# Performance work log

Measured on AMD Instinct MI355X. Metric: run time of the kernel, lower is better.

## Reference

```python
import jax, jax.numpy as jnp
import numpy as np

D_IN = 1024
D_OUT = 1024
NUM_HEADS = 16
HEAD_DIM = D_OUT // NUM_HEADS


def setup_inputs() -> dict:
    key = jax.random.key(0)
    ks = jax.random.split(key, 6)
    s = 1.0 / np.sqrt(D_IN)
    x = jax.random.normal(ks[0], (2, 2048, D_IN), dtype=jnp.float32)
    Wq = jax.random.uniform(ks[1], (D_IN, D_OUT), jnp.float32, -s, s)
    Wk = jax.random.uniform(ks[2], (D_IN, D_OUT), jnp.float32, -s, s)
    Wv = jax.random.uniform(ks[3], (D_IN, D_OUT), jnp.float32, -s, s)
    Wo = jax.random.uniform(ks[4], (D_OUT, D_OUT), jnp.float32, -s, s)
    bo = jax.random.uniform(ks[5], (D_OUT,), jnp.float32, -s, s)
    return {"x": x, "Wq": Wq, "Wk": Wk, "Wv": Wv, "Wo": Wo, "bo": bo}


def reference(x, Wq, Wk, Wv, Wo, bo):
    b, s, _ = x.shape
    # Note: source assigns keys = W_query(x), queries = W_key(x) (swapped names);
    # replicate exactly.
    keys = (x @ Wq).reshape(b, s, NUM_HEADS, HEAD_DIM)
    values = (x @ Wv).reshape(b, s, NUM_HEADS, HEAD_DIM)
    queries = (x @ Wk).reshape(b, s, NUM_HEADS, HEAD_DIM)
    # [b, h, q, k] attention scores; source's masked_fill is non in-place and
    # discarded, so NO causal mask is applied (faithful to the bug).
    scores = jnp.einsum("bqhd,bkhd->bhqk", queries, keys)
    attn = jax.nn.softmax(scores / np.sqrt(HEAD_DIM), axis=-1)
    # dropout p=0.0 -> identity
    ctx = jnp.einsum("bhqk,bkhd->bqhd", attn, values).reshape(b, s, D_OUT)
    return ctx @ Wo + bo
```

## Files before the change

kernel.cpp:

```cpp
#include <hip/hip_runtime.h>
#include <math.h>

#define DI 1024
#define SQ 2048
#define NB 2
#define NH 16
#define HD 64
#define QSCALE 0.18033688f

typedef __attribute__((ext_vector_type(8))) short short8;
typedef __attribute__((ext_vector_type(4))) float f32x4;
typedef __attribute__((ext_vector_type(2))) unsigned int uint2v;
typedef __attribute__((ext_vector_type(4))) int int4v;
typedef __attribute__((ext_vector_type(4))) unsigned short ushort4v;

static __device__ __forceinline__ unsigned short f2bf(float f) {
    union { float f; unsigned u; } v; v.f = f;
    unsigned r = v.u + 0x7FFFu + ((v.u >> 16) & 1u);
    return (unsigned short)(r >> 16);
}
static __device__ __forceinline__ float fexp2(float x) {
    float r; asm("v_exp_f32 %0, %1" : "=v"(r) : "v"(x)); return r;
}
static __device__ __forceinline__ unsigned cvtpk(float lo, float hi) {
    unsigned r; asm("v_cvt_pk_bf16_f32 %0, %1, %2" : "=v"(r) : "v"(lo), "v"(hi)); return r;
}

typedef __attribute__((address_space(1))) const unsigned int gas_uint;
typedef __attribute__((address_space(3))) unsigned int las_uint;
static __device__ __forceinline__ void gload16(const void* g, void* l) {
    __builtin_amdgcn_global_load_lds((gas_uint*)g, (las_uint*)l, 16, 0, 0);
}

#define MFMA16(a, b, c) __builtin_amdgcn_mfma_f32_16x16x32_bf16(a, b, c, 0, 0, 0)

__global__ __launch_bounds__(256) void k_cvt_bf16(const float* __restrict__ src,
                                                  unsigned short* __restrict__ dst) {
    int i = blockIdx.x * 256 + threadIdx.x;
    const f32x4* s4 = (const f32x4*)src + (size_t)i * 2;
    f32x4 a = s4[0], b = s4[1];
    ushort4v o0, o1;
    o0[0] = f2bf(a[0]); o0[1] = f2bf(a[1]); o0[2] = f2bf(a[2]); o0[3] = f2bf(a[3]);
    o1[0] = f2bf(b[0]); o1[1] = f2bf(b[1]); o1[2] = f2bf(b[2]); o1[3] = f2bf(b[3]);
    *(ushort4v*)(dst + (size_t)i * 8)     = o0;
    *(ushort4v*)(dst + (size_t)i * 8 + 4) = o1;
}

__global__ __launch_bounds__(256) void k_transpose_w4(const float* __restrict__ W0, const float* __restrict__ W1,
                                                      const float* __restrict__ W2, const float* __restrict__ W3,
                                                      unsigned short* __restrict__ T0, unsigned short* __restrict__ T1,
                                                      unsigned short* __restrict__ T2, unsigned short* __restrict__ T3) {
    const float* W; unsigned short* T;
    switch (blockIdx.z) {
        case 0: W = W0; T = T0; break;
        case 1: W = W1; T = T1; break;
        case 2: W = W2; T = T2; break;
        default: W = W3; T = T3; break;
    }
    __shared__ float t[32][33];
    int tx = threadIdx.x, ty = threadIdx.y;
    int n0 = blockIdx.x * 32, k0 = blockIdx.y * 32;
#pragma unroll
    for (int j = 0; j < 32; j += 8) t[ty + j][tx] = W[(size_t)(k0 + ty + j) * DI + n0 + tx];
    __syncthreads();
#pragma unroll
    for (int j = 0; j < 32; j += 8)
        T[(size_t)(n0 + ty + j) * DI + k0 + tx] = f2bf(t[tx][ty + j]);
}

template <int MODE>
__global__ __launch_bounds__(256) void k_gemm(const unsigned short* __restrict__ A,
                                              const unsigned short* __restrict__ Bt,
                                              unsigned short* __restrict__ oK,
                                              unsigned short* __restrict__ oQ,
                                              unsigned short* __restrict__ oV,
                                              const float* __restrict__ bias) {
    __shared__ __align__(16) unsigned short As[2][128 * 32];
    __shared__ __align__(16) unsigned short Bs[2][128 * 32];
    const int tid = threadIdx.x, lane = tid & 63, w = tid >> 6;
    const int wr = w >> 1, wc = w & 1;
    const int tm = blockIdx.y, tn = blockIdx.x;
    const unsigned short* Abase = A  + (size_t)tm * 128 * DI;
    const unsigned short* Bbase = Bt + (size_t)tn * 128 * DI;

    auto stage = [&](int kt, int bi) {
#pragma unroll
        for (int i = 0; i < 2; ++i) {
            int u = tid + i * 256;
            int row = u >> 2, c8 = (u & 3) * 8;
            gload16(Abase + (size_t)row * DI + kt * 32 + c8, &As[bi][u * 8]);
            gload16(Bbase + (size_t)row * DI + kt * 32 + c8, &Bs[bi][u * 8]);
        }
    };

    f32x4 acc[4][4] = {};
    stage(0, 0);
    for (int kt = 0; kt < DI / 32; ++kt) {
        __syncthreads();
        if (kt + 1 < DI / 32) stage(kt + 1, (kt + 1) & 1);
        const int bi = kt & 1;
        short8 af[4], bf[4];
#pragma unroll
        for (int mi = 0; mi < 4; ++mi)
            af[mi] = *(const short8*)&As[bi][(wr * 64 + mi * 16 + (lane & 15)) * 32 + (lane >> 4) * 8];
#pragma unroll
        for (int ni = 0; ni < 4; ++ni)
            bf[ni] = *(const short8*)&Bs[bi][(wc * 64 + ni * 16 + (lane & 15)) * 32 + (lane >> 4) * 8];
        __builtin_amdgcn_s_setprio(1);
#pragma unroll
        for (int mi = 0; mi < 4; ++mi)
#pragma unroll
            for (int ni = 0; ni < 4; ++ni)
                acc[mi][ni] = MFMA16(af[mi], bf[ni], acc[mi][ni]);
        __builtin_amdgcn_s_setprio(0);
    }

    if (MODE == 2) {
        float bv[4];
#pragma unroll
        for (int ni = 0; ni < 4; ++ni) bv[ni] = bias[tn * 128 + wc * 64 + ni * 16 + (lane & 15)];
        float* Co = (float*)oK;
#pragma unroll
        for (int mi = 0; mi < 4; ++mi)
#pragma unroll
            for (int ni = 0; ni < 4; ++ni)
#pragma unroll
                for (int j = 0; j < 4; ++j) {
                    int m = tm * 128 + wr * 64 + mi * 16 + (lane >> 4) * 4 + j;
                    int n = tn * 128 + wc * 64 + ni * 16 + (lane & 15);
                    Co[(size_t)m * DI + n] = acc[mi][ni][j] + bv[ni];
                }
    } else {
        const int which = tn >> 3;
        if (which < 2) {
            unsigned short* Co = which ? oQ : oK;
            const float scl = which ? QSCALE : 1.0f;
#pragma unroll
            for (int mi = 0; mi < 4; ++mi)
#pragma unroll
                for (int ni = 0; ni < 4; ++ni)
#pragma unroll
                    for (int j = 0; j < 4; ++j) {
                        int m = tm * 128 + wr * 64 + mi * 16 + (lane >> 4) * 4 + j;
                        int n = (tn & 7) * 128 + wc * 64 + ni * 16 + (lane & 15);
                        Co[(((size_t)(m >> 11) * NH + (n >> 6)) * SQ + (m & 2047)) * HD + (n & 63)] =
                            f2bf(acc[mi][ni][j] * scl);
                    }
        } else {
#pragma unroll
            for (int mi = 0; mi < 4; ++mi)
#pragma unroll
                for (int ni = 0; ni < 4; ++ni) {
                    uint2v pk;
                    pk[0] = cvtpk(acc[mi][ni][0], acc[mi][ni][1]);
                    pk[1] = cvtpk(acc[mi][ni][2], acc[mi][ni][3]);
                    int m = tm * 128 + wr * 64 + mi * 16 + (lane >> 4) * 4;
                    int n = (tn & 7) * 128 + wc * 64 + ni * 16 + (lane & 15);
                    *(uint2v*)&oV[(((size_t)(m >> 11) * NH + (n >> 6)) * HD + (n & 63)) * SQ + (m & 2047)] = pk;
                }
        }
    }
}

__global__ __launch_bounds__(256) void k_attn(const unsigned short* __restrict__ Q,
                                              const unsigned short* __restrict__ K,
                                              const unsigned short* __restrict__ Vt,
                                              unsigned short* __restrict__ ctx) {
    __shared__ __align__(16) unsigned short Ks[2][64 * 64];
    __shared__ __align__(16) unsigned short Vs[2][64 * 64];
    __shared__ __align__(16) unsigned short Ps[4][32 * 64];
    const int tid = threadIdx.x, lane = tid & 63, w = tid >> 6;
    const int bh = blockIdx.y;
    const int q0 = blockIdx.x * 128;
    const unsigned short* qh = Q  + (size_t)bh * SQ * HD;
    const unsigned short* kh = K  + (size_t)bh * SQ * HD;
    const unsigned short* vh = Vt + (size_t)bh * HD * SQ;

    short8 qf[2][2];
#pragma unroll
    for (int mi = 0; mi < 2; ++mi)
#pragma unroll
        for (int kk = 0; kk < 2; ++kk)
            qf[mi][kk] = *(const short8*)(qh + (size_t)(q0 + w * 32 + mi * 16 + (lane & 15)) * HD +
                                          kk * 32 + (lane >> 4) * 8);

    f32x4 o[2][4] = {};
    float ls[2][4] = {};

    auto stage = [&](int kt, int bi) {
#pragma unroll
        for (int i = 0; i < 2; ++i) {
            int u = tid + i * 256;
            int row = u >> 3, c = u & 7;
            int cs = c ^ (row & 7);
            gload16(kh + (size_t)(kt * 64 + row) * HD + cs * 8, &Ks[bi][u * 8]);
            gload16(vh + (size_t)row * SQ + kt * 64 + cs * 8, &Vs[bi][u * 8]);
        }
    };

    stage(0, 0);
    for (int kt = 0; kt < SQ / 64; ++kt) {
        __syncthreads();
        if (kt + 1 < SQ / 64) stage(kt + 1, (kt + 1) & 1);
        const int bi = kt & 1;

        f32x4 s[2][4] = {};
#pragma unroll
        for (int kk = 0; kk < 2; ++kk) {
            short8 kb[4];
#pragma unroll
            for (int ni = 0; ni < 4; ++ni)
                kb[ni] = *(const short8*)&Ks[bi][(ni * 16 + (lane & 15)) * 64 +
                                                 (((kk * 4 + (lane >> 4)) ^ (lane & 7)) * 8)];
            __builtin_amdgcn_s_setprio(1);
#pragma unroll
            for (int mi = 0; mi < 2; ++mi)
#pragma unroll
                for (int ni = 0; ni < 4; ++ni)
                    s[mi][ni] = MFMA16(qf[mi][kk], kb[ni], s[mi][ni]);
            __builtin_amdgcn_s_setprio(0);
        }

#pragma unroll
        for (int mi = 0; mi < 2; ++mi)
#pragma unroll
            for (int ni = 0; ni < 4; ++ni) {
                float p0 = fexp2(s[mi][ni][0]), p1 = fexp2(s[mi][ni][1]);
                float p2 = fexp2(s[mi][ni][2]), p3 = fexp2(s[mi][ni][3]);
                ls[mi][0] += p0; ls[mi][1] += p1; ls[mi][2] += p2; ls[mi][3] += p3;
                unsigned pk01 = cvtpk(p0, p1), pk23 = cvtpk(p2, p3);
                int colc = ni * 2 + ((lane & 15) >> 3);
                int cl = lane & 7;
#pragma unroll
                for (int j = 0; j < 4; ++j) {
                    int row = mi * 16 + (lane >> 4) * 4 + j;
                    unsigned v = (j & 1) ? ((j < 2 ? pk01 : pk23) >> 16)
                                         : (j < 2 ? pk01 : pk23);
                    Ps[w][row * 64 + ((colc ^ (row & 7)) * 8) + cl] = (unsigned short)v;
                }
            }

#pragma unroll
        for (int kk = 0; kk < 2; ++kk) {
            short8 pa[2], vb[4];
#pragma unroll
            for (int mi = 0; mi < 2; ++mi) {
                int row = mi * 16 + (lane & 15);
                pa[mi] = *(const short8*)&Ps[w][row * 64 + (((kk * 4 + (lane >> 4)) ^ (row & 7)) * 8)];
            }
#pragma unroll
            for (int ni = 0; ni < 4; ++ni)
                vb[ni] = *(const short8*)&Vs[bi][(ni * 16 + (lane & 15)) * 64 +
                                                 (((kk * 4 + (lane >> 4)) ^ (lane & 7)) * 8)];
            __builtin_amdgcn_s_setprio(1);
#pragma unroll
            for (int mi = 0; mi < 2; ++mi)
#pragma unroll
                for (int ni = 0; ni < 4; ++ni)
                    o[mi][ni] = MFMA16(pa[mi], vb[ni], o[mi][ni]);
            __builtin_amdgcn_s_setprio(0);
        }
    }

    float inv[2][4];
#pragma unroll
    for (int mi = 0; mi < 2; ++mi)
#pragma unroll
        for (int j = 0; j < 4; ++j) {
            float v = ls[mi][j];
            v += __shfl_xor(v, 1); v += __shfl_xor(v, 2);
            v += __shfl_xor(v, 4); v += __shfl_xor(v, 8);
            inv[mi][j] = 1.0f / v;
        }

    const int b = bh >> 4, h = bh & 15;
#pragma unroll
    for (int mi = 0; mi < 2; ++mi)
#pragma unroll
        for (int ni = 0; ni < 4; ++ni)
#pragma unroll
            for (int j = 0; j < 4; ++j) {
                int q = q0 + w * 32 + mi * 16 + (lane >> 4) * 4 + j;
                int col = h * 64 + ni * 16 + (lane & 15);
                ctx[((size_t)(b * SQ + q)) * DI + col] = f2bf(o[mi][ni][j] * inv[mi][j]);
            }
}

extern "C" void kernel_launch(void* const* d_in, const int* in_sizes, int n_in,
                              void* d_out, int out_size, void* d_ws, size_t ws_size,
                              hipStream_t stream) {
    const float* x  = (const float*)d_in[0];
    const float* Wq = (const float*)d_in[1];
    const float* Wk = (const float*)d_in[2];
    const float* Wv = (const float*)d_in[3];
    const float* Wo = (const float*)d_in[4];
    const float* bo = (const float*)d_in[5];

    char* ws = (char*)d_ws;
    unsigned short* xb   = (unsigned short*)(ws);
    unsigned short* Wall = (unsigned short*)(ws + (8u  << 20));
    unsigned short* Wot  = (unsigned short*)(ws + (14u << 20));
    unsigned short* Qh   = (unsigned short*)(ws + (16u << 20));
    unsigned short* Kh   = (unsigned short*)(ws + (24u << 20));
    unsigned short* Vt   = (unsigned short*)(ws + (32u << 20));
    unsigned short* ctx  = (unsigned short*)(ws + (40u << 20));

    k_cvt_bf16<<<2048, 256, 0, stream>>>(x, xb);
    k_transpose_w4<<<dim3(32, 32, 4), dim3(32, 8), 0, stream>>>(
        Wq, Wk, Wv, Wo, Wall, Wall + (1u << 20), Wall + (2u << 20), Wot);

    k_gemm<0><<<dim3(24, 32), 256, 0, stream>>>(xb, Wall, Kh, Qh, Vt, nullptr);

    k_attn<<<dim3(16, 32), 256, 0, stream>>>(Qh, Kh, Vt, ctx);

    k_gemm<2><<<dim3(8, 32), 256, 0, stream>>>(ctx, Wot, (unsigned short*)d_out, nullptr, nullptr, bo);
}
```

Before: 134.6 us.

## Rewrite attention with 32x32 MFMA, register-resident P via permlane swap

The attention kernel now uses 32x32x16 bf16 MFMAs and computes S transposed (K as A operand), so the exponentiated probabilities can be repacked into the PV operand in registers using v_permlane32_swap instead of round-tripping through a per-wave LDS P buffer. The row-sum reduction shrinks to one cross-half shuffle. Output is staged through LDS for coalesced 16-byte ctx stores, and the 1D grid is remapped so consecutive blocks spread across heads, likely for XCD/L2 locality. This removes LDS writes and reads of P and scattered 2-byte global stores, at the cost of more complex lane mapping and register pressure from 16-wide accumulators.

```diff
diff --git a/kernel.cpp b/kernel.cpp
--- a/kernel.cpp
+++ b/kernel.cpp
@@ -10,6 +10,7 @@
 
 typedef __attribute__((ext_vector_type(8))) short short8;
 typedef __attribute__((ext_vector_type(4))) float f32x4;
+typedef __attribute__((ext_vector_type(16))) float f32x16;
 typedef __attribute__((ext_vector_type(2))) unsigned int uint2v;
 typedef __attribute__((ext_vector_type(4))) int int4v;
 typedef __attribute__((ext_vector_type(4))) unsigned short ushort4v;
@@ -25,6 +26,12 @@
 static __device__ __forceinline__ unsigned cvtpk(float lo, float hi) {
     unsigned r; asm("v_cvt_pk_bf16_f32 %0, %1, %2" : "=v"(r) : "v"(lo), "v"(hi)); return r;
 }
+static __device__ __forceinline__ void plswap(unsigned& a, unsigned& b) {
+    asm volatile("v_permlane32_swap_b32 %0, %1" : "+v"(a), "+v"(b));
+}
+static __device__ __forceinline__ short8 pack4(unsigned a, unsigned b, unsigned c, unsigned d) {
+    union { unsigned u[4]; short8 s; } x; x.u[0] = a; x.u[1] = b; x.u[2] = c; x.u[3] = d; return x.s;
+}
 
 typedef __attribute__((address_space(1))) const unsigned int gas_uint;
 typedef __attribute__((address_space(3))) unsigned int las_uint;
@@ -33,6 +40,7 @@
 }
 
 #define MFMA16(a, b, c) __builtin_amdgcn_mfma_f32_16x16x32_bf16(a, b, c, 0, 0, 0)
+#define MFMA32(a, b, c) __builtin_amdgcn_mfma_f32_32x32x16_bf16(a, b, c, 0, 0, 0)
 
 __global__ __launch_bounds__(256) void k_cvt_bf16(const float* __restrict__ src,
                                                   unsigned short* __restrict__ dst) {
@@ -166,26 +174,27 @@
                                               const unsigned short* __restrict__ K,
                                               const unsigned short* __restrict__ Vt,
                                               unsigned short* __restrict__ ctx) {
-    __shared__ __align__(16) unsigned short Ks[2][64 * 64];
-    __shared__ __align__(16) unsigned short Vs[2][64 * 64];
-    __shared__ __align__(16) unsigned short Ps[4][32 * 64];
+    __shared__ __align__(16) unsigned short smem[16384];
+    unsigned short* Ks = smem;
+    unsigned short* Vs = smem + 8192;
     const int tid = threadIdx.x, lane = tid & 63, w = tid >> 6;
-    const int bh = blockIdx.y;
-    const int q0 = blockIdx.x * 128;
+    const int hi = lane >> 5, l31 = lane & 31;
+
+    const int wg = (blockIdx.x & 7) * 64 + (blockIdx.x >> 3);
+    const int bh = wg >> 4;
+    const int q0 = (wg & 15) * 128;
+
     const unsigned short* qh = Q  + (size_t)bh * SQ * HD;
     const unsigned short* kh = K  + (size_t)bh * SQ * HD;
     const unsigned short* vh = Vt + (size_t)bh * HD * SQ;
 
-    short8 qf[2][2];
-#pragma unroll
-    for (int mi = 0; mi < 2; ++mi)
-#pragma unroll
-        for (int kk = 0; kk < 2; ++kk)
-            qf[mi][kk] = *(const short8*)(qh + (size_t)(q0 + w * 32 + mi * 16 + (lane & 15)) * HD +
-                                          kk * 32 + (lane >> 4) * 8);
-
-    f32x4 o[2][4] = {};
-    float ls[2][4] = {};
+    short8 qf[4];
+#pragma unroll
+    for (int ks = 0; ks < 4; ++ks)
+        qf[ks] = *(const short8*)(qh + (size_t)(q0 + w * 32 + l31) * HD + ks * 16 + hi * 8);
+
+    f32x16 o[2] = {{0}, {0}};
+    float ls = 0.0f;
 
     auto stage = [&](int kt, int bi) {
 #pragma unroll
@@ -193,8 +202,8 @@
             int u = tid + i * 256;
             int row = u >> 3, c = u & 7;
             int cs = c ^ (row & 7);
-            gload16(kh + (size_t)(kt * 64 + row) * HD + cs * 8, &Ks[bi][u * 8]);
-            gload16(vh + (size_t)row * SQ + kt * 64 + cs * 8, &Vs[bi][u * 8]);
+            gload16(kh + (size_t)(kt * 64 + row) * HD + cs * 8, Ks + bi * 4096 + u * 8);
+            gload16(vh + (size_t)row * SQ + kt * 64 + cs * 8, Vs + bi * 4096 + u * 8);
         }
     };
 
@@ -202,88 +211,80 @@
     for (int kt = 0; kt < SQ / 64; ++kt) {
         __syncthreads();
         if (kt + 1 < SQ / 64) stage(kt + 1, (kt + 1) & 1);
-        const int bi = kt & 1;
-
-        f32x4 s[2][4] = {};
-#pragma unroll
-        for (int kk = 0; kk < 2; ++kk) {
-            short8 kb[4];
-#pragma unroll
-            for (int ni = 0; ni < 4; ++ni)
-                kb[ni] = *(const short8*)&Ks[bi][(ni * 16 + (lane & 15)) * 64 +
-                                                 (((kk * 4 + (lane >> 4)) ^ (lane & 7)) * 8)];
+        const unsigned short* kb_ = Ks + (kt & 1) * 4096;
+        const unsigned short* vb_ = Vs + (kt & 1) * 4096;
+
+#pragma unroll
+        for (int kb = 0; kb < 2; ++kb) {
+            f32x16 s = {};
+            {
+                short8 kf[4];
+#pragma unroll
+                for (int ks = 0; ks < 4; ++ks) {
+                    int row = kb * 32 + l31;
+                    kf[ks] = *(const short8*)&kb_[row * 64 + (((ks * 2 + hi) ^ (row & 7)) * 8)];
+                }
+                __builtin_amdgcn_s_setprio(1);
+#pragma unroll
+                for (int ks = 0; ks < 4; ++ks) s = MFMA32(kf[ks], qf[ks], s);
+                __builtin_amdgcn_s_setprio(0);
+            }
+
+            float p[16];
+#pragma unroll
+            for (int r = 0; r < 16; ++r) { p[r] = fexp2(s[r]); ls += p[r]; }
+
+            unsigned g0 = cvtpk(p[0],  p[1]),  g1 = cvtpk(p[2],  p[3]);
+            unsigned g2 = cvtpk(p[4],  p[5]),  g3 = cvtpk(p[6],  p[7]);
+            unsigned g4 = cvtpk(p[8],  p[9]),  g5 = cvtpk(p[10], p[11]);
+            unsigned g6 = cvtpk(p[12], p[13]), g7 = cvtpk(p[14], p[15]);
+            plswap(g0, g2); plswap(g1, g3);
+            plswap(g4, g6); plswap(g5, g7);
+            short8 pf[2] = { pack4(g0, g1, g2, g3), pack4(g4, g5, g6, g7) };
+
+            short8 vf[2][2];
+#pragma unroll
+            for (int ks2 = 0; ks2 < 2; ++ks2)
+#pragma unroll
+                for (int da = 0; da < 2; ++da) {
+                    int row = da * 32 + l31;
+                    vf[ks2][da] = *(const short8*)&vb_[row * 64 + (((kb * 4 + ks2 * 2 + hi) ^ (row & 7)) * 8)];
+                }
             __builtin_amdgcn_s_setprio(1);
 #pragma unroll
-            for (int mi = 0; mi < 2; ++mi)
-#pragma unroll
-                for (int ni = 0; ni < 4; ++ni)
-                    s[mi][ni] = MFMA16(qf[mi][kk], kb[ni], s[mi][ni]);
+            for (int ks2 = 0; ks2 < 2; ++ks2)
+#pragma unroll
+                for (int da = 0; da < 2; ++da)
+                    o[da] = MFMA32(vf[ks2][da], pf[ks2], o[da]);
             __builtin_amdgcn_s_setprio(0);
         }
-
-#pragma unroll
-        for (int mi = 0; mi < 2; ++mi)
-#pragma unroll
-            for (int ni = 0; ni < 4; ++ni) {
-                float p0 = fexp2(s[mi][ni][0]), p1 = fexp2(s[mi][ni][1]);
-                float p2 = fexp2(s[mi][ni][2]), p3 = fexp2(s[mi][ni][3]);
-                ls[mi][0] += p0; ls[mi][1] += p1; ls[mi][2] += p2; ls[mi][3] += p3;
-                unsigned pk01 = cvtpk(p0, p1), pk23 = cvtpk(p2, p3);
-                int colc = ni * 2 + ((lane & 15) >> 3);
-                int cl = lane & 7;
-#pragma unroll
-                for (int j = 0; j < 4; ++j) {
-                    int row = mi * 16 + (lane >> 4) * 4 + j;
-                    unsigned v = (j & 1) ? ((j < 2 ? pk01 : pk23) >> 16)
-                                         : (j < 2 ? pk01 : pk23);
-                    Ps[w][row * 64 + ((colc ^ (row & 7)) * 8) + cl] = (unsigned short)v;
-                }
-            }
-
-#pragma unroll
-        for (int kk = 0; kk < 2; ++kk) {
-            short8 pa[2], vb[4];
-#pragma unroll
-            for (int mi = 0; mi < 2; ++mi) {
-                int row = mi * 16 + (lane & 15);
-                pa[mi] = *(const short8*)&Ps[w][row * 64 + (((kk * 4 + (lane >> 4)) ^ (row & 7)) * 8)];
-            }
-#pragma unroll
-            for (int ni = 0; ni < 4; ++ni)
-                vb[ni] = *(const short8*)&Vs[bi][(ni * 16 + (lane & 15)) * 64 +
-                                                 (((kk * 4 + (lane >> 4)) ^ (lane & 7)) * 8)];
-            __builtin_amdgcn_s_setprio(1);
-#pragma unroll
-            for (int mi = 0; mi < 2; ++mi)
-#pragma unroll
-                for (int ni = 0; ni < 4; ++ni)
-                    o[mi][ni] = MFMA16(pa[mi], vb[ni], o[mi][ni]);
-            __builtin_amdgcn_s_setprio(0);
-        }
-    }
-
-    float inv[2][4];
-#pragma unroll
-    for (int mi = 0; mi < 2; ++mi)
-#pragma unroll
-        for (int j = 0; j < 4; ++j) {
-            float v = ls[mi][j];
-            v += __shfl_xor(v, 1); v += __shfl_xor(v, 2);
-            v += __shfl_xor(v, 4); v += __shfl_xor(v, 8);
-            inv[mi][j] = 1.0f / v;
-        }
+    }
+
+    __syncthreads();
+
+    float dsum = ls + __shfl_xor(ls, 32);
+    float inv = 1.0f / dsum;
+
+    unsigned short* osc = smem + w * 2304;
+#pragma unroll
+    for (int da = 0; da < 2; ++da)
+#pragma unroll
+        for (int g = 0; g < 4; ++g) {
+            uint2v pk;
+            pk[0] = cvtpk(o[da][4 * g]     * inv, o[da][4 * g + 1] * inv);
+            pk[1] = cvtpk(o[da][4 * g + 2] * inv, o[da][4 * g + 3] * inv);
+            int d = da * 32 + 8 * g + 4 * hi;
+            *(uint2v*)&osc[l31 * 72 + d] = pk;
+        }
+    __syncthreads();
 
     const int b = bh >> 4, h = bh & 15;
 #pragma unroll
-    for (int mi = 0; mi < 2; ++mi)
-#pragma unroll
-        for (int ni = 0; ni < 4; ++ni)
-#pragma unroll
-            for (int j = 0; j < 4; ++j) {
-                int q = q0 + w * 32 + mi * 16 + (lane >> 4) * 4 + j;
-                int col = h * 64 + ni * 16 + (lane & 15);
-                ctx[((size_t)(b * SQ + q)) * DI + col] = f2bf(o[mi][ni][j] * inv[mi][j]);
-            }
+    for (int rr = 0; rr < 4; ++rr) {
+        int qrow = rr * 8 + (lane >> 3), ck = lane & 7;
+        int4v vv = *(const int4v*)&osc[qrow * 72 + ck * 8];
+        *(int4v*)&ctx[((size_t)(b * SQ + q0 + w * 32 + qrow)) * DI + h * 64 + ck * 8] = vv;
+    }
 }
 
 extern "C" void kernel_launch(void* const* d_in, const int* in_sizes, int n_in,
@@ -311,7 +312,7 @@
 
     k_gemm<0><<<dim3(24, 32), 256, 0, stream>>>(xb, Wall, Kh, Qh, Vt, nullptr);
 
-    k_attn<<<dim3(16, 32), 256, 0, stream>>>(Qh, Kh, Vt, ctx);
+    k_attn<<<dim3(512), 256, 0, stream>>>(Qh, Kh, Vt, ctx);
 
     k_gemm<2><<<dim3(8, 32), 256, 0, stream>>>(ctx, Wot, (unsigned short*)d_out, nullptr, nullptr, bo);
 }
```

New measurement: 122.3 us. 1.1x faster.
